# Optimization experiments

Measured on AMD Instinct MI355X. Metric: run time of the kernel, lower is better.

The kernel has to match this reference:

```python
import jax, jax.numpy as jnp
import numpy as np

B, T, IN, D = 32, 1024, 1536, 768


def setup_inputs() -> dict:
    key = jax.random.key(0)
    ks = jax.random.split(key, 14)
    s_in = 1.0 / np.sqrt(IN)
    s_d = 1.0 / np.sqrt(D)
    return {
        "x": jax.random.normal(ks[0], (B, T, IN), jnp.float32),
        # fc1/fc2 torch Linear weights stored [out, in]
        "fc1_w": jax.random.normal(ks[1], (IN, IN), jnp.float32) * s_in,
        "fc1_b": jax.random.normal(ks[2], (IN,), jnp.float32) * 0.01,
        "fc2_w": jax.random.normal(ks[3], (D, IN), jnp.float32) * s_in,
        "fc2_b": jax.random.normal(ks[4], (D,), jnp.float32) * 0.01,
        # Unary: Conv1d(D,D,k=1) then Conv1d(D,1,k=1); k=1 conv == per-token linear
        "un_emb_w": jax.random.normal(ks[5], (D, D), jnp.float32) * s_d,
        "un_emb_b": jax.random.normal(ks[6], (D,), jnp.float32) * 0.01,
        "un_red_w": jax.random.normal(ks[7], (1, D), jnp.float32) * s_d,
        "un_red_b": jax.random.normal(ks[8], (1,), jnp.float32) * 0.01,
        # Self Pairwise: x_embedding / y_embedding Conv1d(D,D,k=1)
        "pw_x_w": jax.random.normal(ks[9], (D, D), jnp.float32) * s_d,
        "pw_x_b": jax.random.normal(ks[10], (D,), jnp.float32) * 0.01,
        "pw_y_w": jax.random.normal(ks[11], (D, D), jnp.float32) * s_d,
        "pw_y_b": jax.random.normal(ks[12], (D,), jnp.float32) * 0.01,
        # reduce_potentials: Conv1d(2,1,k=1,bias=False) -> 2 scalars
        "red_w": jax.random.normal(ks[13], (2,), jnp.float32),
    }


def reference(x, fc1_w, fc1_b, fc2_w, fc2_b,
              un_emb_w, un_emb_b, un_red_w, un_red_b,
              pw_x_w, pw_x_b, pw_y_w, pw_y_b, red_w):
    # FGAEmbedder MLP: fc2(relu(fc1(x)))
    h = jax.nn.relu(jnp.einsum('bti,oi->bto', x, fc1_w) + fc1_b)
    u = jnp.einsum('bti,oi->bto', h, fc2_w) + fc2_b            # [B,T,D]

    # Unary potential (dropout is identity at inference)
    e = jax.nn.relu(jnp.einsum('btd,od->bto', u, un_emb_w) + un_emb_b)
    un_pot = (jnp.einsum('btd,od->bto', e, un_red_w) + un_red_b)[..., 0]  # [B,T]

    # Self pairwise: cosine-similarity matrix, marginalized by mean (spatial_dim=None)
    xe = jnp.einsum('btd,od->bto', u, pw_x_w) + pw_x_b
    ye = jnp.einsum('btd,od->bto', u, pw_y_w) + pw_y_b
    xn = xe / jnp.maximum(jnp.linalg.norm(xe, axis=-1, keepdims=True), 1e-12)
    yn = ye / jnp.maximum(jnp.linalg.norm(ye, axis=-1, keepdims=True), 1e-12)
    S = jnp.einsum('btd,bsd->bts', xn, yn)                     # [B,T,T]
    pw_pot = jnp.mean(S, axis=2)                               # [B,T]

    # reduce potentials (Conv1d 2->1 no bias; order: unary then self), softmax attention
    scores = red_w[0] * un_pot + red_w[1] * pw_pot             # [B,T]
    w = jax.nn.softmax(scores, axis=1)
    return jnp.einsum('btd,bt->bd', u, w)                      # [B,D]
```

## Files before the change

kernel.cpp:

```cpp
#include <hip/hip_runtime.h>
#include <stdint.h>

#define MROWS 32768
#define TSEQ  1024
#define BBATCH 32
#define INDIM 1536
#define DDIM  768
#define NCAT  2304

typedef short short8 __attribute__((ext_vector_type(8)));
typedef short short4v __attribute__((ext_vector_type(4)));
typedef float f32x4  __attribute__((ext_vector_type(4)));

__device__ __forceinline__ float b2f(ushort u) {
    union { uint32_t u; float f; } x; x.u = ((uint32_t)u) << 16; return x.f;
}
__device__ __forceinline__ ushort f2b(float f) {
    union { float f; uint32_t u; } x; x.f = f;
    uint32_t r = x.u + 0x7fffu + ((x.u >> 16) & 1u);
    return (ushort)(r >> 16);
}

__device__ __forceinline__ void cvt4(const float* __restrict__ in, ushort* __restrict__ out, int i) {
    float4 v = ((const float4*)in)[i];
    ushort4 o;
    o.x = f2b(v.x); o.y = f2b(v.y); o.z = f2b(v.z); o.w = f2b(v.w);
    ((ushort4*)out)[i] = o;
}

#define C0 12582912
#define C1 13172736
#define C2 13467648
#define C3 13615104
#define C4 13762560
#define C5 13910016
#define C6 13910592
#define C7 13916736
#define C8 13922880
#define C9 13947456
__global__ void cvt_all(const float* __restrict__ x,
                        const float* __restrict__ fc1_w, const float* __restrict__ fc2_w,
                        const float* __restrict__ w3a, const float* __restrict__ w3b,
                        const float* __restrict__ w3c,
                        const float* __restrict__ ba, const float* __restrict__ bb,
                        const float* __restrict__ bc,
                        ushort* __restrict__ X16, ushort* __restrict__ W1,
                        ushort* __restrict__ W2, ushort* __restrict__ W3,
                        float* __restrict__ B3, float* __restrict__ ybar_z,
                        float* __restrict__ out_z, float* __restrict__ stats_z)
{
    int i = blockIdx.x * 256 + threadIdx.x;
    float4 z = {0.f, 0.f, 0.f, 0.f};
    if (i < C0)       cvt4(x, X16, i);
    else if (i < C1)  cvt4(fc1_w, W1, i - C0);
    else if (i < C2)  cvt4(fc2_w, W2, i - C1);
    else if (i < C3)  cvt4(w3a, W3,           i - C2);
    else if (i < C4)  cvt4(w3b, W3 + 589824,  i - C3);
    else if (i < C5)  cvt4(w3c, W3 + 1179648, i - C4);
    else if (i < C6) {
        int j = i - C5;
        const float* src = (j < 192) ? ba : (j < 384) ? bb : bc;
        int off = (j < 192) ? j : (j < 384) ? (j - 192) : (j - 384);
        ((float4*)B3)[j] = ((const float4*)src)[off];
    }
    else if (i < C7)  ((float4*)ybar_z)[i - C6] = z;
    else if (i < C8)  ((float4*)out_z)[i - C7] = z;
    else if (i < C9)  ((float4*)stats_z)[i - C8] = z;
}

__global__ __launch_bounds__(512, 2)
void gemm_bt(const ushort* __restrict__ A, const ushort* __restrict__ Bm,
             const float* __restrict__ bias, ushort* __restrict__ C,
             int M, int N, int K, int relu_ncols,
             const float* __restrict__ urw, float* __restrict__ SE,
             float* __restrict__ SX, float* __restrict__ SY)
{
    __shared__ __align__(16) ushort lds[81920];

    const int tid  = threadIdx.x;
    const int lane = tid & 63, wave = tid >> 6;
    const int wm = wave >> 2, wn = wave & 3;
    const int quad = lane >> 4, r16 = lane & 15;

    const int ntiles = N >> 8;
    const int xcd = blockIdx.x & 7;
    const int j   = blockIdx.x >> 3;
    const int g   = j / ntiles;
    const int n_t = j - g * ntiles;
    const int m_t = xcd + (g << 3);
    const int m0 = m_t * 256, n0 = n_t * 256;

    const int srow = lane >> 2;
    const int g8   = (((lane & 3) ^ ((srow >> 1) & 3)) << 3);
    const int goff = (r16 << 5) + ((quad ^ ((r16 >> 1) & 3)) << 3);

    const ushort* pA = A + (size_t)(m0 + (wave & 3) * 16 + srow + (wave >> 2) * 128) * K + g8;
    const int segA = (((wave >> 2) * 8 + (wave & 3)) << 9) + lane * 8;
    const ushort* pB = Bm + (size_t)(n0 + (wave >> 1) * 64 + (wave & 1) * 16 + srow) * K + g8;
    const int segB = (((wave >> 1) * 4 + (wave & 1)) << 9) + lane * 8;

    const int kT = K >> 6;

#define STG(p, off) __builtin_amdgcn_global_load_lds( \
        (const __attribute__((address_space(1))) void*)(p), \
        (__attribute__((address_space(3))) void*)&lds[off], 16, 0, 0)
#define STAGE_A(tt, MH) do { \
        const ushort* s_ = pA + (size_t)(MH) * 64 * K + (size_t)(tt) * 64; \
        const int d_ = ((tt) % 3) * 16384 + (MH) * 2048 + segA; \
        STG(s_,      d_); \
        STG(s_ + 32, d_ + 8192); } while (0)
#define STAGE_B(tt, NH) do { \
        const ushort* s_ = pB + (size_t)(NH) * 32 * K + (size_t)(tt) * 64; \
        const int d_ = 49152 + ((tt) & 1) * 16384 + (NH) * 1024 + segB; \
        STG(s_,      d_); \
        STG(s_ + 32, d_ + 8192); } while (0)

    STAGE_A(0, 0); STAGE_A(0, 1);
    STAGE_B(0, 0); STAGE_B(0, 1);
    STAGE_A(1, 0); STAGE_A(1, 1);
    asm volatile("s_waitcnt vmcnt(4)" ::: "memory");
    asm volatile("s_barrier" ::: "memory");

    f32x4 acc[8][4] = {};
    short8 af0[2][4], af1[2][4], bf[2][2];

    for (int t = 0; t < kT; ++t) {
        const int aB = (t % 3) * 16384;
        const int bB = 49152 + (t & 1) * 16384;
        const bool stB = (t + 1 < kT), stA = (t + 2 < kT);

#pragma unroll
        for (int ks = 0; ks < 2; ++ks) {
#pragma unroll
            for (int i = 0; i < 4; ++i)
                af0[ks][i] = *(const short8*)&lds[aB + ks * 8192 + (wm * 8 + i) * 512 + goff];
#pragma unroll
            for (int jj = 0; jj < 2; ++jj)
                bf[ks][jj] = *(const short8*)&lds[bB + ks * 8192 + (wn * 4 + jj) * 512 + goff];
        }
        if (stB) STAGE_B(t + 1, 0);
        asm volatile("s_barrier" ::: "memory");
        asm volatile("s_waitcnt lgkmcnt(0)" ::: "memory");
        __builtin_amdgcn_s_setprio(1);
#pragma unroll
        for (int i = 0; i < 4; ++i)
#pragma unroll
            for (int jj = 0; jj < 2; ++jj) {
                acc[i][jj] = __builtin_amdgcn_mfma_f32_16x16x32_bf16(af0[0][i], bf[0][jj], acc[i][jj], 0, 0, 0);
                acc[i][jj] = __builtin_amdgcn_mfma_f32_16x16x32_bf16(af0[1][i], bf[1][jj], acc[i][jj], 0, 0, 0);
            }
        __builtin_amdgcn_s_setprio(0);
        asm volatile("s_barrier" ::: "memory");

#pragma unroll
        for (int ks = 0; ks < 2; ++ks)
#pragma unroll
            for (int i = 0; i < 4; ++i)
                af1[ks][i] = *(const short8*)&lds[aB + ks * 8192 + (wm * 8 + 4 + i) * 512 + goff];
        if (stB) STAGE_B(t + 1, 1);
        asm volatile("s_barrier" ::: "memory");
        asm volatile("s_waitcnt lgkmcnt(0)" ::: "memory");
        __builtin_amdgcn_s_setprio(1);
#pragma unroll
        for (int i = 0; i < 4; ++i)
#pragma unroll
            for (int jj = 0; jj < 2; ++jj) {
                acc[4 + i][jj] = __builtin_amdgcn_mfma_f32_16x16x32_bf16(af1[0][i], bf[0][jj], acc[4 + i][jj], 0, 0, 0);
                acc[4 + i][jj] = __builtin_amdgcn_mfma_f32_16x16x32_bf16(af1[1][i], bf[1][jj], acc[4 + i][jj], 0, 0, 0);
            }
        __builtin_amdgcn_s_setprio(0);
        asm volatile("s_barrier" ::: "memory");

#pragma unroll
        for (int ks = 0; ks < 2; ++ks)
#pragma unroll
            for (int jj = 0; jj < 2; ++jj)
                bf[ks][jj] = *(const short8*)&lds[bB + ks * 8192 + (wn * 4 + 2 + jj) * 512 + goff];
        if (stA) STAGE_A(t + 2, 0);
        asm volatile("s_barrier" ::: "memory");
        asm volatile("s_waitcnt lgkmcnt(0)" ::: "memory");
        __builtin_amdgcn_s_setprio(1);
#pragma unroll
        for (int i = 0; i < 4; ++i)
#pragma unroll
            for (int jj = 0; jj < 2; ++jj) {
                acc[4 + i][2 + jj] = __builtin_amdgcn_mfma_f32_16x16x32_bf16(af1[0][i], bf[0][jj], acc[4 + i][2 + jj], 0, 0, 0);
                acc[4 + i][2 + jj] = __builtin_amdgcn_mfma_f32_16x16x32_bf16(af1[1][i], bf[1][jj], acc[4 + i][2 + jj], 0, 0, 0);
            }
        __builtin_amdgcn_s_setprio(0);
        asm volatile("s_barrier" ::: "memory");

        if (stA) STAGE_A(t + 2, 1);
        if (t + 3 <= kT)      asm volatile("s_waitcnt vmcnt(4)" ::: "memory");
        else if (t == kT - 2) asm volatile("s_waitcnt vmcnt(0)" ::: "memory");
        asm volatile("s_barrier" ::: "memory");
        __builtin_amdgcn_s_setprio(1);
#pragma unroll
        for (int i = 0; i < 4; ++i)
#pragma unroll
            for (int jj = 0; jj < 2; ++jj) {
                acc[i][2 + jj] = __builtin_amdgcn_mfma_f32_16x16x32_bf16(af0[0][i], bf[0][jj], acc[i][2 + jj], 0, 0, 0);
                acc[i][2 + jj] = __builtin_amdgcn_mfma_f32_16x16x32_bf16(af0[1][i], bf[1][jj], acc[i][2 + jj], 0, 0, 0);
            }
        __builtin_amdgcn_s_setprio(0);
        asm volatile("s_barrier" ::: "memory");
    }
#undef STAGE_A
#undef STAGE_B
#undef STG

    const bool stats = (urw != nullptr);
    const int sec = n0 / DDIM;
    float bv[4], uwv[4];
    bool dr[4];
#pragma unroll
    for (int jj = 0; jj < 4; ++jj) {
        int gn = n0 + wn * 64 + jj * 16 + r16;
        bv[jj] = bias[gn];
        dr[jj] = gn < relu_ncols;
        uwv[jj] = (stats && sec == 0) ? urw[gn] : 0.f;
    }
    float st[8][4] = {};
#pragma unroll
    for (int i = 0; i < 8; ++i) {
#pragma unroll
        for (int rr = 0; rr < 4; ++rr) {
            size_t base = (size_t)(m0 + wm * 128 + i * 16 + quad * 4 + rr) * N + n0 + wn * 64 + r16;
#pragma unroll
            for (int jj = 0; jj < 4; ++jj) {
                float v = acc[i][jj][rr] + bv[jj];
                if (dr[jj]) v = fmaxf(v, 0.f);
                C[base + jj * 16] = f2b(v);
                if (stats) st[i][rr] += (sec == 0) ? v * uwv[jj] : v * v;
            }
        }
    }
    if (stats) {
#pragma unroll
        for (int i = 0; i < 8; ++i)
#pragma unroll
            for (int rr = 0; rr < 4; ++rr) {
                float v = st[i][rr];
                v += __shfl_xor(v, 1, 64);
                v += __shfl_xor(v, 2, 64);
                v += __shfl_xor(v, 4, 64);
                v += __shfl_xor(v, 8, 64);
                st[i][rr] = v;
            }
        if (r16 == 0) {
            float* dst = (sec == 0) ? SE : (sec == 1) ? SX : SY;
#pragma unroll
            for (int i = 0; i < 8; ++i)
#pragma unroll
                for (int rr = 0; rr < 4; ++rr)
                    atomicAdd(&dst[m0 + wm * 128 + i * 16 + quad * 4 + rr], st[i][rr]);
        }
    }
}

__global__ void ybar_k(const ushort* __restrict__ G3, const float* __restrict__ sy,
                       float* __restrict__ ybar)
{
    int b = blockIdx.x, s0 = blockIdx.y * 32;
    int tid = threadIdx.x;
    __shared__ float sr[32];
    if (tid < 32) {
        float v = sy[b * TSEQ + s0 + tid];
        sr[tid] = (1.0f / TSEQ) / fmaxf(sqrtf(v), 1e-12f);
    }
    __syncthreads();
    float a0 = 0.f, a1 = 0.f, a2 = 0.f;
#pragma unroll 8
    for (int s = 0; s < 32; ++s) {
        const ushort* row = G3 + (size_t)(b * TSEQ + s0 + s) * NCAT + 2 * DDIM;
        float w = sr[s];
        a0 += b2f(row[tid])       * w;
        a1 += b2f(row[tid + 256]) * w;
        a2 += b2f(row[tid + 512]) * w;
    }
    atomicAdd(&ybar[b * DDIM + tid],       a0);
    atomicAdd(&ybar[b * DDIM + tid + 256], a1);
    atomicAdd(&ybar[b * DDIM + tid + 512], a2);
}

__global__ void pw_scores_k(const ushort* __restrict__ G3, const float* __restrict__ ybar,
                            const float* __restrict__ SE, const float* __restrict__ SX,
                            const float* __restrict__ urb, const float* __restrict__ red_w,
                            float* __restrict__ scores)
{
    int wv = threadIdx.x >> 6, lane = threadIdx.x & 63;
    int m = blockIdx.x * 4 + wv;
    int b = m >> 10;
    const ushort* xe = G3 + (size_t)m * NCAT + DDIM;
    const float4* yb = (const float4*)(ybar + b * DDIM);
    float s = 0.f;
#pragma unroll
    for (int c0 = 0; c0 < 3; ++c0) {
        int c = lane + c0 * 64;
        short4v v = *(const short4v*)(xe + c * 4);
        float4 yv = yb[c];
        s += b2f((ushort)v[0]) * yv.x + b2f((ushort)v[1]) * yv.y
           + b2f((ushort)v[2]) * yv.z + b2f((ushort)v[3]) * yv.w;
    }
#pragma unroll
    for (int off = 32; off; off >>= 1) s += __shfl_xor(s, off, 64);
    if (lane == 0) {
        float rnx = 1.f / fmaxf(sqrtf(SX[m]), 1e-12f);
        scores[m] = red_w[0] * (SE[m] + urb[0]) + red_w[1] * (rnx * s);
    }
}

__global__ void out_sm_k(const ushort* __restrict__ U16, const float* __restrict__ scores,
                         float* __restrict__ out)
{
    int b = blockIdx.x, t0 = blockIdx.y * 32;
    int tid = threadIdx.x;
    int lane = tid & 63, wv = tid >> 6;
    __shared__ float red[8];
    __shared__ float sw[32];

    float v[4];
    float lm = -1e30f;
#pragma unroll
    for (int i = 0; i < 4; ++i) {
        v[i] = scores[b * TSEQ + i * 256 + tid];
        lm = fmaxf(lm, v[i]);
    }
#pragma unroll
    for (int off = 32; off; off >>= 1) lm = fmaxf(lm, __shfl_xor(lm, off, 64));
    if (lane == 0) red[wv] = lm;
    __syncthreads();
    float smax = fmaxf(fmaxf(red[0], red[1]), fmaxf(red[2], red[3]));
    float ls = 0.f;
#pragma unroll
    for (int i = 0; i < 4; ++i) ls += expf(v[i] - smax);
#pragma unroll
    for (int off = 32; off; off >>= 1) ls += __shfl_xor(ls, off, 64);
    if (lane == 0) red[4 + wv] = ls;
    __syncthreads();
    float inv = 1.f / (red[4] + red[5] + red[6] + red[7]);

    if (tid < 32) sw[tid] = expf(scores[b * TSEQ + t0 + tid] - smax) * inv;
    __syncthreads();

    float a0 = 0.f, a1 = 0.f, a2 = 0.f;
#pragma unroll 8
    for (int t = 0; t < 32; ++t) {
        const ushort* row = U16 + (size_t)(b * TSEQ + t0 + t) * DDIM;
        float w = sw[t];
        a0 += b2f(row[tid])       * w;
        a1 += b2f(row[tid + 256]) * w;
        a2 += b2f(row[tid + 512]) * w;
    }
    atomicAdd(&out[b * DDIM + tid],       a0);
    atomicAdd(&out[b * DDIM + tid + 256], a1);
    atomicAdd(&out[b * DDIM + tid + 512], a2);
}

static const size_t O_X16   = 0;
static const size_t O_H16   = 100663296;
static const size_t O_G3    = 0;
static const size_t O_U16   = 201326592;
static const size_t O_W1    = 251658240;
static const size_t O_W2    = 256376832;
static const size_t O_W3    = 258736128;
static const size_t O_B3    = 262275072;
static const size_t O_SE    = 262284288;
static const size_t O_SX    = 262415360;
static const size_t O_SY    = 262546432;
static const size_t O_SCORE = 262677504;
static const size_t O_YBAR  = 262939648;

extern "C" void kernel_launch(void* const* d_in, const int* in_sizes, int n_in,
                              void* d_out, int out_size, void* d_ws, size_t ws_size,
                              hipStream_t stream)
{
    const float* x        = (const float*)d_in[0];
    const float* fc1_w    = (const float*)d_in[1];
    const float* fc1_b    = (const float*)d_in[2];
    const float* fc2_w    = (const float*)d_in[3];
    const float* fc2_b    = (const float*)d_in[4];
    const float* un_emb_w = (const float*)d_in[5];
    const float* un_emb_b = (const float*)d_in[6];
    const float* un_red_w = (const float*)d_in[7];
    const float* un_red_b = (const float*)d_in[8];
    const float* pw_x_w   = (const float*)d_in[9];
    const float* pw_x_b   = (const float*)d_in[10];
    const float* pw_y_w   = (const float*)d_in[11];
    const float* pw_y_b   = (const float*)d_in[12];
    const float* red_w    = (const float*)d_in[13];

    char* ws = (char*)d_ws;
    ushort* X16 = (ushort*)(ws + O_X16);
    ushort* H16 = (ushort*)(ws + O_H16);
    ushort* G3  = (ushort*)(ws + O_G3);
    ushort* U16 = (ushort*)(ws + O_U16);
    ushort* W1  = (ushort*)(ws + O_W1);
    ushort* W2  = (ushort*)(ws + O_W2);
    ushort* W3  = (ushort*)(ws + O_W3);
    float*  B3  = (float*)(ws + O_B3);
    float*  SE  = (float*)(ws + O_SE);
    float*  SX  = (float*)(ws + O_SX);
    float*  SY  = (float*)(ws + O_SY);
    float*  SCORES = (float*)(ws + O_SCORE);
    float*  YBAR = (float*)(ws + O_YBAR);

    cvt_all<<<54483, 256, 0, stream>>>(x, fc1_w, fc2_w, un_emb_w, pw_x_w, pw_y_w,
                                       un_emb_b, pw_x_b, pw_y_b,
                                       X16, W1, W2, W3, B3, YBAR, (float*)d_out, SE);

    gemm_bt<<<(MROWS / 256) * (INDIM / 256), 512, 0, stream>>>(
        X16, W1, fc1_b, H16, MROWS, INDIM, INDIM, INDIM,
        nullptr, nullptr, nullptr, nullptr);
    gemm_bt<<<(MROWS / 256) * (DDIM / 256), 512, 0, stream>>>(
        H16, W2, fc2_b, U16, MROWS, DDIM, INDIM, 0,
        nullptr, nullptr, nullptr, nullptr);
    gemm_bt<<<(MROWS / 256) * (NCAT / 256), 512, 0, stream>>>(
        U16, W3, B3, G3, MROWS, NCAT, DDIM, DDIM,
        un_red_w, SE, SX, SY);

    ybar_k<<<dim3(BBATCH, 32), 256, 0, stream>>>(G3, SY, YBAR);
    pw_scores_k<<<MROWS / 4, 256, 0, stream>>>(G3, YBAR, SE, SX, un_red_b, red_w, SCORES);
    out_sm_k<<<dim3(BBATCH, 32), 256, 0, stream>>>(U16, SCORES, (float*)d_out);
}
```

Baseline: 733.5 us.

## Load GEMM B operand directly into registers and cut LDS staging barriers

The main GEMM loop no longer stages the B (weight) tile through LDS. Each wave now loads its 64 B columns straight from global memory into double-buffered registers, prefetching one k-step ahead. Only A stays in a triple-buffered LDS ring, which shrinks LDS use and reduces the loop to one barrier per k-step instead of several. In exchange, the two waves that share a column slice both load the same B data, doubling B reads from L2, and the extra register buffers may raise register pressure or cause spills under the 512x2 launch bounds.

```diff
diff --git a/kernel.cpp b/kernel.cpp
--- a/kernel.cpp
+++ b/kernel.cpp
@@ -75,7 +75,7 @@
              const float* __restrict__ urw, float* __restrict__ SE,
              float* __restrict__ SX, float* __restrict__ SY)
 {
-    __shared__ __align__(16) ushort lds[81920];
+    __shared__ __align__(16) ushort lds[49152];
 
     const int tid  = threadIdx.x;
     const int lane = tid & 63, wave = tid >> 6;
@@ -96,8 +96,8 @@
 
     const ushort* pA = A + (size_t)(m0 + (wave & 3) * 16 + srow + (wave >> 2) * 128) * K + g8;
     const int segA = (((wave >> 2) * 8 + (wave & 3)) << 9) + lane * 8;
-    const ushort* pB = Bm + (size_t)(n0 + (wave >> 1) * 64 + (wave & 1) * 16 + srow) * K + g8;
-    const int segB = (((wave >> 1) * 4 + (wave & 1)) << 9) + lane * 8;
+
+    const ushort* pBg = Bm + (size_t)(n0 + wn * 64 + r16) * K + quad * 8;
 
     const int kT = K >> 6;
 
@@ -109,104 +109,54 @@
         const int d_ = ((tt) % 3) * 16384 + (MH) * 2048 + segA; \
         STG(s_,      d_); \
         STG(s_ + 32, d_ + 8192); } while (0)
-#define STAGE_B(tt, NH) do { \
-        const ushort* s_ = pB + (size_t)(NH) * 32 * K + (size_t)(tt) * 64; \
-        const int d_ = 49152 + ((tt) & 1) * 16384 + (NH) * 1024 + segB; \
-        STG(s_,      d_); \
-        STG(s_ + 32, d_ + 8192); } while (0)
 
     STAGE_A(0, 0); STAGE_A(0, 1);
-    STAGE_B(0, 0); STAGE_B(0, 1);
     STAGE_A(1, 0); STAGE_A(1, 1);
-    asm volatile("s_waitcnt vmcnt(4)" ::: "memory");
+    f32x4 acc[8][4] = {};
+    short8 bfA[2][4], bfB[2][4];
+#pragma unroll
+    for (int ks = 0; ks < 2; ++ks)
+#pragma unroll
+        for (int j2 = 0; j2 < 4; ++j2)
+            bfA[ks][j2] = *(const short8*)(pBg + (size_t)(j2 * 16) * K + ks * 32);
+    asm volatile("s_waitcnt vmcnt(0)" ::: "memory");
     asm volatile("s_barrier" ::: "memory");
 
-    f32x4 acc[8][4] = {};
-    short8 af0[2][4], af1[2][4], bf[2][2];
-
-    for (int t = 0; t < kT; ++t) {
-        const int aB = (t % 3) * 16384;
-        const int bB = 49152 + (t & 1) * 16384;
-        const bool stB = (t + 1 < kT), stA = (t + 2 < kT);
-
-#pragma unroll
-        for (int ks = 0; ks < 2; ++ks) {
-#pragma unroll
-            for (int i = 0; i < 4; ++i)
-                af0[ks][i] = *(const short8*)&lds[aB + ks * 8192 + (wm * 8 + i) * 512 + goff];
-#pragma unroll
-            for (int jj = 0; jj < 2; ++jj)
-                bf[ks][jj] = *(const short8*)&lds[bB + ks * 8192 + (wn * 4 + jj) * 512 + goff];
-        }
-        if (stB) STAGE_B(t + 1, 0);
-        asm volatile("s_barrier" ::: "memory");
-        asm volatile("s_waitcnt lgkmcnt(0)" ::: "memory");
-        __builtin_amdgcn_s_setprio(1);
-#pragma unroll
-        for (int i = 0; i < 4; ++i)
-#pragma unroll
-            for (int jj = 0; jj < 2; ++jj) {
-                acc[i][jj] = __builtin_amdgcn_mfma_f32_16x16x32_bf16(af0[0][i], bf[0][jj], acc[i][jj], 0, 0, 0);
-                acc[i][jj] = __builtin_amdgcn_mfma_f32_16x16x32_bf16(af0[1][i], bf[1][jj], acc[i][jj], 0, 0, 0);
-            }
-        __builtin_amdgcn_s_setprio(0);
-        asm volatile("s_barrier" ::: "memory");
-
-#pragma unroll
-        for (int ks = 0; ks < 2; ++ks)
-#pragma unroll
-            for (int i = 0; i < 4; ++i)
-                af1[ks][i] = *(const short8*)&lds[aB + ks * 8192 + (wm * 8 + 4 + i) * 512 + goff];
-        if (stB) STAGE_B(t + 1, 1);
-        asm volatile("s_barrier" ::: "memory");
-        asm volatile("s_waitcnt lgkmcnt(0)" ::: "memory");
-        __builtin_amdgcn_s_setprio(1);
-#pragma unroll
-        for (int i = 0; i < 4; ++i)
-#pragma unroll
-            for (int jj = 0; jj < 2; ++jj) {
-                acc[4 + i][jj] = __builtin_amdgcn_mfma_f32_16x16x32_bf16(af1[0][i], bf[0][jj], acc[4 + i][jj], 0, 0, 0);
-                acc[4 + i][jj] = __builtin_amdgcn_mfma_f32_16x16x32_bf16(af1[1][i], bf[1][jj], acc[4 + i][jj], 0, 0, 0);
-            }
-        __builtin_amdgcn_s_setprio(0);
-        asm volatile("s_barrier" ::: "memory");
-
-#pragma unroll
-        for (int ks = 0; ks < 2; ++ks)
-#pragma unroll
-            for (int jj = 0; jj < 2; ++jj)
-                bf[ks][jj] = *(const short8*)&lds[bB + ks * 8192 + (wn * 4 + 2 + jj) * 512 + goff];
-        if (stA) STAGE_A(t + 2, 0);
-        asm volatile("s_barrier" ::: "memory");
-        asm volatile("s_waitcnt lgkmcnt(0)" ::: "memory");
-        __builtin_amdgcn_s_setprio(1);
-#pragma unroll
-        for (int i = 0; i < 4; ++i)
-#pragma unroll
-            for (int jj = 0; jj < 2; ++jj) {
-                acc[4 + i][2 + jj] = __builtin_amdgcn_mfma_f32_16x16x32_bf16(af1[0][i], bf[0][jj], acc[4 + i][2 + jj], 0, 0, 0);
-                acc[4 + i][2 + jj] = __builtin_amdgcn_mfma_f32_16x16x32_bf16(af1[1][i], bf[1][jj], acc[4 + i][2 + jj], 0, 0, 0);
-            }
-        __builtin_amdgcn_s_setprio(0);
-        asm volatile("s_barrier" ::: "memory");
-
-        if (stA) STAGE_A(t + 2, 1);
-        if (t + 3 <= kT)      asm volatile("s_waitcnt vmcnt(4)" ::: "memory");
-        else if (t == kT - 2) asm volatile("s_waitcnt vmcnt(0)" ::: "memory");
-        asm volatile("s_barrier" ::: "memory");
-        __builtin_amdgcn_s_setprio(1);
-#pragma unroll
-        for (int i = 0; i < 4; ++i)
-#pragma unroll
-            for (int jj = 0; jj < 2; ++jj) {
-                acc[i][2 + jj] = __builtin_amdgcn_mfma_f32_16x16x32_bf16(af0[0][i], bf[0][jj], acc[i][2 + jj], 0, 0, 0);
-                acc[i][2 + jj] = __builtin_amdgcn_mfma_f32_16x16x32_bf16(af0[1][i], bf[1][jj], acc[i][2 + jj], 0, 0, 0);
-            }
-        __builtin_amdgcn_s_setprio(0);
-        asm volatile("s_barrier" ::: "memory");
-    }
+#define ITER(t, bfc, bfn) do { \
+    const int aB_ = ((t) % 3) * 16384; \
+    short8 af0_[2][4], af1_[2][4]; \
+    _Pragma("unroll") for (int ks_ = 0; ks_ < 2; ++ks_) \
+    _Pragma("unroll") for (int i_ = 0; i_ < 4; ++i_) \
+        af0_[ks_][i_] = *(const short8*)&lds[aB_ + ks_ * 8192 + (wm * 8 + i_) * 512 + goff]; \
+    if ((t) + 2 < kT) { STAGE_A((t) + 2, 0); STAGE_A((t) + 2, 1); } \
+    if ((t) + 1 < kT) { \
+        _Pragma("unroll") for (int ks_ = 0; ks_ < 2; ++ks_) \
+        _Pragma("unroll") for (int j_ = 0; j_ < 4; ++j_) \
+            bfn[ks_][j_] = *(const short8*)(pBg + (size_t)(j_ * 16) * K + ((t) + 1) * 64 + ks_ * 32); } \
+    __builtin_amdgcn_s_setprio(1); \
+    _Pragma("unroll") for (int i_ = 0; i_ < 4; ++i_) \
+    _Pragma("unroll") for (int j_ = 0; j_ < 4; ++j_) { \
+        acc[i_][j_] = __builtin_amdgcn_mfma_f32_16x16x32_bf16(af0_[0][i_], bfc[0][j_], acc[i_][j_], 0, 0, 0); \
+        acc[i_][j_] = __builtin_amdgcn_mfma_f32_16x16x32_bf16(af0_[1][i_], bfc[1][j_], acc[i_][j_], 0, 0, 0); } \
+    _Pragma("unroll") for (int ks_ = 0; ks_ < 2; ++ks_) \
+    _Pragma("unroll") for (int i_ = 0; i_ < 4; ++i_) \
+        af1_[ks_][i_] = *(const short8*)&lds[aB_ + ks_ * 8192 + (wm * 8 + 4 + i_) * 512 + goff]; \
+    _Pragma("unroll") for (int i_ = 0; i_ < 4; ++i_) \
+    _Pragma("unroll") for (int j_ = 0; j_ < 4; ++j_) { \
+        acc[4 + i_][j_] = __builtin_amdgcn_mfma_f32_16x16x32_bf16(af1_[0][i_], bfc[0][j_], acc[4 + i_][j_], 0, 0, 0); \
+        acc[4 + i_][j_] = __builtin_amdgcn_mfma_f32_16x16x32_bf16(af1_[1][i_], bfc[1][j_], acc[4 + i_][j_], 0, 0, 0); } \
+    __builtin_amdgcn_s_setprio(0); \
+    if ((t) + 2 < kT)      asm volatile("s_waitcnt vmcnt(12)" ::: "memory"); \
+    else if ((t) + 1 < kT) asm volatile("s_waitcnt vmcnt(8)" ::: "memory"); \
+    if ((t) + 1 < kT)      asm volatile("s_barrier" ::: "memory"); \
+} while (0)
+
+    for (int t = 0; t < kT; t += 2) {
+        ITER(t,     bfA, bfB);
+        ITER(t + 1, bfB, bfA);
+    }
+#undef ITER
 #undef STAGE_A
-#undef STAGE_B
 #undef STG
 
     const bool stats = (urw != nullptr);
```

Measured after the change: 894.0 us. 21.9% more time.

## Collapse GEMM main loop into one barrier per K-tile with up-front staging

Applied to the files above, without the earlier changes.

Restructures the GEMM K-loop. Each iteration now loads all four B fragments into registers at once, issues all global-to-LDS staging for the next B tile and the tile after for A at the top, then runs two MFMA phases. The per-phase barriers, lgkmcnt waits and the second B-fragment reload are gone, leaving a single vmcnt wait plus one barrier per iteration. This cuts synchronisation overhead and lets the MFMAs be scheduled more freely, at the cost of more live fragment registers and less interleaving of staging traffic with compute.

```diff
diff --git a/kernel.cpp b/kernel.cpp
--- a/kernel.cpp
+++ b/kernel.cpp
@@ -122,12 +122,11 @@
     asm volatile("s_barrier" ::: "memory");
 
     f32x4 acc[8][4] = {};
-    short8 af0[2][4], af1[2][4], bf[2][2];
 
     for (int t = 0; t < kT; ++t) {
         const int aB = (t % 3) * 16384;
         const int bB = 49152 + (t & 1) * 16384;
-        const bool stB = (t + 1 < kT), stA = (t + 2 < kT);
+        short8 af0[2][4], af1[2][4], bf[2][4];
 
 #pragma unroll
         for (int ks = 0; ks < 2; ++ks) {
@@ -135,75 +134,41 @@
             for (int i = 0; i < 4; ++i)
                 af0[ks][i] = *(const short8*)&lds[aB + ks * 8192 + (wm * 8 + i) * 512 + goff];
 #pragma unroll
-            for (int jj = 0; jj < 2; ++jj)
+            for (int jj = 0; jj < 4; ++jj)
                 bf[ks][jj] = *(const short8*)&lds[bB + ks * 8192 + (wn * 4 + jj) * 512 + goff];
         }
-        if (stB) STAGE_B(t + 1, 0);
-        asm volatile("s_barrier" ::: "memory");
-        asm volatile("s_waitcnt lgkmcnt(0)" ::: "memory");
+        if (t + 1 < kT) { STAGE_B(t + 1, 0); STAGE_B(t + 1, 1); }
+        if (t + 2 < kT) { STAGE_A(t + 2, 0); STAGE_A(t + 2, 1); }
+
         __builtin_amdgcn_s_setprio(1);
 #pragma unroll
         for (int i = 0; i < 4; ++i)
 #pragma unroll
-            for (int jj = 0; jj < 2; ++jj) {
+            for (int jj = 0; jj < 4; ++jj) {
                 acc[i][jj] = __builtin_amdgcn_mfma_f32_16x16x32_bf16(af0[0][i], bf[0][jj], acc[i][jj], 0, 0, 0);
                 acc[i][jj] = __builtin_amdgcn_mfma_f32_16x16x32_bf16(af0[1][i], bf[1][jj], acc[i][jj], 0, 0, 0);
             }
         __builtin_amdgcn_s_setprio(0);
-        asm volatile("s_barrier" ::: "memory");
 
 #pragma unroll
         for (int ks = 0; ks < 2; ++ks)
 #pragma unroll
             for (int i = 0; i < 4; ++i)
                 af1[ks][i] = *(const short8*)&lds[aB + ks * 8192 + (wm * 8 + 4 + i) * 512 + goff];
-        if (stB) STAGE_B(t + 1, 1);
-        asm volatile("s_barrier" ::: "memory");
-        asm volatile("s_waitcnt lgkmcnt(0)" ::: "memory");
+
         __builtin_amdgcn_s_setprio(1);
 #pragma unroll
         for (int i = 0; i < 4; ++i)
 #pragma unroll
-            for (int jj = 0; jj < 2; ++jj) {
+            for (int jj = 0; jj < 4; ++jj) {
                 acc[4 + i][jj] = __builtin_amdgcn_mfma_f32_16x16x32_bf16(af1[0][i], bf[0][jj], acc[4 + i][jj], 0, 0, 0);
                 acc[4 + i][jj] = __builtin_amdgcn_mfma_f32_16x16x32_bf16(af1[1][i], bf[1][jj], acc[4 + i][jj], 0, 0, 0);
             }
         __builtin_amdgcn_s_setprio(0);
-        asm volatile("s_barrier" ::: "memory");
-
-#pragma unroll
-        for (int ks = 0; ks < 2; ++ks)
-#pragma unroll
-            for (int jj = 0; jj < 2; ++jj)
-                bf[ks][jj] = *(const short8*)&lds[bB + ks * 8192 + (wn * 4 + 2 + jj) * 512 + goff];
-        if (stA) STAGE_A(t + 2, 0);
-        asm volatile("s_barrier" ::: "memory");
-        asm volatile("s_waitcnt lgkmcnt(0)" ::: "memory");
-        __builtin_amdgcn_s_setprio(1);
-#pragma unroll
-        for (int i = 0; i < 4; ++i)
-#pragma unroll
-            for (int jj = 0; jj < 2; ++jj) {
-                acc[4 + i][2 + jj] = __builtin_amdgcn_mfma_f32_16x16x32_bf16(af1[0][i], bf[0][jj], acc[4 + i][2 + jj], 0, 0, 0);
-                acc[4 + i][2 + jj] = __builtin_amdgcn_mfma_f32_16x16x32_bf16(af1[1][i], bf[1][jj], acc[4 + i][2 + jj], 0, 0, 0);
-            }
-        __builtin_amdgcn_s_setprio(0);
-        asm volatile("s_barrier" ::: "memory");
-
-        if (stA) STAGE_A(t + 2, 1);
-        if (t + 3 <= kT)      asm volatile("s_waitcnt vmcnt(4)" ::: "memory");
-        else if (t == kT - 2) asm volatile("s_waitcnt vmcnt(0)" ::: "memory");
-        asm volatile("s_barrier" ::: "memory");
-        __builtin_amdgcn_s_setprio(1);
-#pragma unroll
-        for (int i = 0; i < 4; ++i)
-#pragma unroll
-            for (int jj = 0; jj < 2; ++jj) {
-                acc[i][2 + jj] = __builtin_amdgcn_mfma_f32_16x16x32_bf16(af0[0][i], bf[0][jj], acc[i][2 + jj], 0, 0, 0);
-                acc[i][2 + jj] = __builtin_amdgcn_mfma_f32_16x16x32_bf16(af0[1][i], bf[1][jj], acc[i][2 + jj], 0, 0, 0);
-            }
-        __builtin_amdgcn_s_setprio(0);
-        asm volatile("s_barrier" ::: "memory");
+
+        if (t + 2 < kT)      asm volatile("s_waitcnt vmcnt(4)" ::: "memory");
+        else if (t + 1 < kT) asm volatile("s_waitcnt vmcnt(0)" ::: "memory");
+        if (t + 1 < kT)      asm volatile("s_barrier" ::: "memory");
     }
 #undef STAGE_A
 #undef STAGE_B
```

Result: faster. 700.3 us (-4.5%).
